# Performance work log

Measured on AMD Instinct MI355X. Metric: run time of the kernel, lower is better.

The kernel has to match this reference:

```python
import jax, jax.numpy as jnp
import numpy as np

B = 8            # graphs per batch
N_PER = 32768    # nodes per graph (equal-size graphs -> trivial to_dense_batch)
N = B * N_PER    # total nodes
DEG = 8
E = N * DEG      # total edges
D = 64           # hidden dim (hard-coded 64 in the module)
K = 16           # num_clusters
NCT = 8          # n_cell_type_groups


def setup_inputs() -> dict:
    key = jax.random.key(0)
    ks = jax.random.split(key, 12)
    # node cell-type indices (x[:,0].long() feeds the embedding)
    x = jax.random.randint(ks[0], (N, 1), 0, NCT, dtype=jnp.int32)
    # within-graph edges: graph id of edge e is e // (E//B)
    epg = E // B
    g = jnp.arange(E, dtype=jnp.int64) // epg
    src = jax.random.randint(ks[1], (E,), 0, N_PER, dtype=jnp.int64) + g * N_PER
    dst = jax.random.randint(ks[2], (E,), 0, N_PER, dtype=jnp.int64) + g * N_PER
    edge_index = jnp.stack([src, dst], axis=0)
    batch = (jnp.arange(N, dtype=jnp.int32) // N_PER).astype(jnp.int32)
    n_cells = jnp.full((B,), float(N_PER), dtype=jnp.float32)
    # parameters
    def lin(k, fi, fo):
        kw, kb = jax.random.split(k)
        lim = 1.0 / np.sqrt(fi)
        return (jax.random.uniform(kw, (fi, fo), jnp.float32, -lim, lim),
                jax.random.uniform(kb, (fo,), jnp.float32, -lim, lim))
    emb_w = jax.random.normal(ks[3], (NCT, D), jnp.float32) * (np.sqrt(6.0 / (NCT + D)) / np.sqrt(3.0))
    W2, b2 = lin(ks[4], D, D)   # conv2 (GCNConv 64->64)
    W3, b3 = lin(ks[5], D, D)   # conv3 (GCNConv 64->64)
    W1, b1 = lin(ks[6], D, K)   # linear1 -> cluster logits
    Wp, bp = lin(ks[7], K, 1)   # linear2 ('prop' head)
    return {"x": x, "edge_index": edge_index, "batch": batch, "n_cells": n_cells,
            "emb_w": emb_w, "W2": W2, "b2": b2, "W3": W3, "b3": b3,
            "W1": W1, "b1": b1, "Wp": Wp, "bp": bp}


def _forward(x, edge_index, batch, n_cells, emb_w, W2, b2, W3, b3, W1, b1, Wp, bp):
    n = x.shape[0]
    h = emb_w[x[:, 0]]                                   # [N, 64] embedding lookup
    src, dst = edge_index[0], edge_index[1]
    # GCN normalization with self-loops
    ar = jnp.arange(n, dtype=src.dtype)
    src_sl = jnp.concatenate([src, ar])
    dst_sl = jnp.concatenate([dst, ar])
    deg = jax.ops.segment_sum(jnp.ones_like(dst_sl, dtype=h.dtype), dst_sl, num_segments=n)
    dis = jax.lax.rsqrt(deg)                             # deg >= 1 (self-loops)
    norm = dis[src_sl] * dis[dst_sl]                     # [E+N]

    def gcn(z, W, b):
        m = z @ W                                        # [N, Dout]
        msg = m[src_sl] * norm[:, None]                  # gather + scale
        return jax.ops.segment_sum(msg, dst_sl, num_segments=n) + b

    # n_gcns == 2, skip_type == 'no'
    out = jax.nn.relu(gcn(h, W2, b2))
    out = jax.nn.relu(gcn(out, W3, b3))
    s = out @ W1 + b1                                    # [N, K] cluster logits
    s_soft = jax.nn.softmax(s, axis=-1)

    # sparse mincut pooling losses
    g_e = batch[src].astype(jnp.int32)                   # graph id per edge
    mincut_num = jax.ops.segment_sum((s_soft[src] * s_soft[dst]).sum(-1), g_e, num_segments=B)
    deg_a = jax.ops.segment_sum(jnp.ones((src.shape[0],), h.dtype), src, num_segments=n)
    mincut_den = jax.ops.segment_sum(deg_a * (s_soft * s_soft).sum(-1), batch, num_segments=B)
    mc1 = jnp.mean(-mincut_num / mincut_den)

    s_b = s_soft.reshape(B, N_PER, K)                    # to_dense_batch (equal graphs)
    SS = jnp.einsum('bnk,bnl->bkl', s_b, s_b)            # [B, K, K]
    ss_norm = jnp.sqrt(jnp.sum(SS * SS, axis=(-2, -1), keepdims=True))
    i_k = jnp.eye(K, dtype=h.dtype) / jnp.sqrt(jnp.asarray(K, h.dtype))
    diff = SS / ss_norm - i_k
    o1 = jnp.mean(jnp.sqrt(jnp.sum(diff * diff, axis=(-2, -1))))

    # predictor_type == 'prop'
    xp = s_b.sum(axis=-2) / n_cells[:, None]             # [B, K]
    pred = xp @ Wp + bp                                  # [B, 1]
    return pred, s_b, mc1, o1


def reference(x, edge_index, batch, n_cells, emb_w, W2, b2, W3, b3, W1, b1, Wp, bp):
    return _forward(x, edge_index, batch, n_cells, emb_w, W2, b2, W3, b3, W1, b1, Wp, bp)
```

## Files before the change

kernel.cpp:

```cpp
#include <hip/hip_runtime.h>
#include <hip/hip_bf16.h>
#include <hip/hip_fp16.h>
#include <math.h>

#define NN 262144
#define EE 2097152
#define NPER 32768
#define EPG 262144
#define EMAX 5120

typedef float4 f4;
typedef __attribute__((ext_vector_type(4))) float f32x4;
typedef __attribute__((ext_vector_type(8))) _Float16 half8;
typedef __attribute__((ext_vector_type(4))) _Float16 half4;

__global__ __launch_bounds__(256) void k_hist(const int* __restrict__ ei, int* __restrict__ histT) {
  __shared__ int histl[64];
  int t = threadIdx.x;
  int bid = blockIdx.x;
  int g = bid & 7, c = bid >> 3;
  if (t < 64) histl[t] = 0;
  __syncthreads();
  int gN = g * NPER;
  const int4* dst4 = (const int4*)(ei + EE + (size_t)g * EPG + c * 4096);
#pragma unroll
  for (int j = 0; j < 4; ++j) {
    int4 d4 = dst4[j * 256 + t];
    atomicAdd(&histl[(d4.x - gN) >> 9], 1);
    atomicAdd(&histl[(d4.y - gN) >> 9], 1);
    atomicAdd(&histl[(d4.z - gN) >> 9], 1);
    atomicAdd(&histl[(d4.w - gN) >> 9], 1);
  }
  __syncthreads();
  if (t < 64) histT[((size_t)g * 64 + t) * 64 + c] = histl[t];
}

__global__ __launch_bounds__(64) void k_hscan(const int* __restrict__ histT, int* __restrict__ winOff,
                                              int* __restrict__ winCnt, int* __restrict__ baseB) {
  int g = blockIdx.x, w = threadIdx.x;
  const int* hrow = histT + ((size_t)g * 64 + w) * 64;
  int tot = 0;
#pragma unroll
  for (int c = 0; c < 64; ++c) tot += hrow[c];
  int incl = tot;
#pragma unroll
  for (int o = 1; o < 64; o <<= 1) {
    int u = __shfl_up(incl, o);
    if (w >= o) incl += u;
  }
  int excl = incl - tot;
  int base = g * EPG + excl;
  winOff[g * 64 + w] = base;
  winCnt[g * 64 + w] = tot;
  int run = base;
  for (int c = 0; c < 64; ++c) {
    baseB[((size_t)g * 64 + c) * 64 + w] = run;
    run += hrow[c];
  }
}

__global__ __launch_bounds__(256) void k_scat(const int* __restrict__ ei, const int* __restrict__ baseB,
                                              int* __restrict__ binned) {
  __shared__ int curl[64];
  int t = threadIdx.x;
  int bid = blockIdx.x;
  int g = bid & 7, c = bid >> 3;
  if (t < 64) curl[t] = baseB[((size_t)g * 64 + c) * 64 + t];
  __syncthreads();
  int gN = g * NPER;
  const int4* src4 = (const int4*)(ei + (size_t)g * EPG + c * 4096);
  const int4* dst4 = (const int4*)(ei + EE + (size_t)g * EPG + c * 4096);
#pragma unroll
  for (int j = 0; j < 4; ++j) {
    int4 s4 = src4[j * 256 + t];
    int4 d4 = dst4[j * 256 + t];
    int dl, w, pos;
    dl = d4.x - gN; w = dl >> 9; pos = atomicAdd(&curl[w], 1); binned[pos] = s4.x | ((dl & 511) << 18);
    dl = d4.y - gN; w = dl >> 9; pos = atomicAdd(&curl[w], 1); binned[pos] = s4.y | ((dl & 511) << 18);
    dl = d4.z - gN; w = dl >> 9; pos = atomicAdd(&curl[w], 1); binned[pos] = s4.z | ((dl & 511) << 18);
    dl = d4.w - gN; w = dl >> 9; pos = atomicAdd(&curl[w], 1); binned[pos] = s4.w | ((dl & 511) << 18);
  }
}

__global__ __launch_bounds__(512) void k_build(const int* __restrict__ binned, const int* __restrict__ winOff,
                                               const int* __restrict__ winCnt, const int* __restrict__ x,
                                               int* __restrict__ offs, int* __restrict__ cnt,
                                               float* __restrict__ dis, float2* __restrict__ dx,
                                               int* __restrict__ adj) {
  __shared__ int ebuf[EMAX];
  __shared__ int cntl[512];
  __shared__ int wsum[8];
  int t = threadIdx.x;
  int bid = blockIdx.x;
  int g = bid & 7, w = bid >> 3;
  int winIdx = g * 64 + w;
  int base = winOff[winIdx];
  int nE = winCnt[winIdx];
  if (nE > EMAX) nE = EMAX;
  for (int i = t; i < nE; i += 512) ebuf[i] = binned[base + i];
  cntl[t] = 0;
  __syncthreads();
  for (int i = t; i < nE; i += 512) atomicAdd(&cntl[ebuf[i] >> 18], 1);
  __syncthreads();
  int c = cntl[t];
  int lane = t & 63, wv = t >> 6;
  int incl = c;
#pragma unroll
  for (int o = 1; o < 64; o <<= 1) {
    int u = __shfl_up(incl, o);
    if (lane >= o) incl += u;
  }
  if (lane == 63) wsum[wv] = incl;
  __syncthreads();
  if (t == 0) {
    int r = 0;
#pragma unroll
    for (int i = 0; i < 8; ++i) { int v = wsum[i]; wsum[i] = r; r += v; }
  }
  __syncthreads();
  int ex = incl - c + wsum[wv];
  int node = g * NPER + w * 512 + t;
  offs[node] = base + ex;
  cnt[node] = c;
  float dn = rsqrtf((float)(c + 1));
  dis[node] = dn;
  dx[node] = make_float2(dn, __int_as_float(x[node]));
  cntl[t] = base + ex;
  __syncthreads();
  for (int i = t; i < nE; i += 512) {
    int v = ebuf[i];
    int pos = atomicAdd(&cntl[v >> 18], 1);
    adj[pos] = v & 0x3FFFF;
  }
}

__global__ void k_m1(const float* __restrict__ emb, const float* __restrict__ W2, float* __restrict__ M1) {
  int t = threadIdx.x;
  int c = t >> 6, j = t & 63;
  float acc = 0.f;
  for (int k = 0; k < 64; ++k) acc += emb[c * 64 + k] * W2[k * 64 + j];
  M1[c * 64 + j] = acc;
}

__global__ __launch_bounds__(256) void k_pack(const float* __restrict__ W3, const float* __restrict__ W1,
                                              _Float16* __restrict__ W3p, _Float16* __restrict__ W1p) {
  int t = blockIdx.x * 256 + threadIdx.x;
  if (t < 4096) {
    int jt = t >> 10, kk = (t >> 9) & 1, l = (t >> 3) & 63, i = t & 7;
    int k = kk * 32 + (l >> 4) * 8 + i;
    int j = jt * 16 + (l & 15);
    W3p[t] = (_Float16)W3[k * 64 + j];
  } else if (t < 5120) {
    int q = t - 4096;
    int kk = q >> 9, l = (q >> 3) & 63, i = q & 7;
    int k = kk * 32 + (l >> 4) * 8 + i;
    int c = l & 15;
    W1p[q] = (_Float16)W1[k * 16 + c];
  }
}

__global__ __launch_bounds__(256) void k_out1(const int* __restrict__ adj, const int* __restrict__ offs,
                                              const int* __restrict__ cnt, const float2* __restrict__ dx,
                                              const float* __restrict__ M1, const float* __restrict__ b2,
                                              __half2* __restrict__ out1h) {
  int tid = threadIdx.x;
  int bid = blockIdx.x;
  int swz = (bid & 7) * 2048 + (bid >> 3);
  int node = swz * 16 + (tid >> 4);
  int t16 = tid & 15;
  float2 dxn = dx[node];
  float dn = dxn.x;
  int xc = __float_as_int(dxn.y);
  int off = offs[node], c = cnt[node];
  float wv[8] = {0.f, 0.f, 0.f, 0.f, 0.f, 0.f, 0.f, 0.f};
  for (int it = t16; it < c; it += 16) {
    int s = adj[off + it];
    float2 v = dx[s];
    int cls = __float_as_int(v.y);
#pragma unroll
    for (int k = 0; k < 8; ++k) wv[k] += (cls == k) ? v.x : 0.f;
  }
#pragma unroll
  for (int k = 0; k < 8; ++k) {
#pragma unroll
    for (int m = 1; m < 16; m <<= 1) wv[k] += __shfl_xor(wv[k], m);
    wv[k] = (wv[k] + ((k == xc) ? dn : 0.f)) * dn;
  }
  int j0 = t16 * 4;
  float o0 = b2[j0], o1 = b2[j0 + 1], o2 = b2[j0 + 2], o3 = b2[j0 + 3];
#pragma unroll
  for (int k = 0; k < 8; ++k) {
    f4 m = *(const f4*)&M1[k * 64 + j0];
    o0 += wv[k] * m.x; o1 += wv[k] * m.y; o2 += wv[k] * m.z; o3 += wv[k] * m.w;
  }
  __half2 h01 = __floats2half2_rn(fmaxf(o0, 0.f) * dn, fmaxf(o1, 0.f) * dn);
  __half2 h23 = __floats2half2_rn(fmaxf(o2, 0.f) * dn, fmaxf(o3, 0.f) * dn);
  size_t p = (size_t)node * 32 + t16 * 2;
  out1h[p] = h01;
  out1h[p + 1] = h23;
}

__global__ __launch_bounds__(256) void k_layer2(const int* __restrict__ adj, const int* __restrict__ offs,
                                                const int* __restrict__ cnt, const float* __restrict__ dis,
                                                const __half2* __restrict__ out1h,
                                                const _Float16* __restrict__ W3p, const float* __restrict__ b3,
                                                const _Float16* __restrict__ W1p, const float* __restrict__ b1,
                                                float* __restrict__ dout) {
  __shared__ _Float16 aggh[16 * 64];
  __shared__ _Float16 o2h[16 * 64];
  int tid = threadIdx.x;
  int bid = blockIdx.x;
  int swz = (bid & 7) * 2048 + (bid >> 3);
  int lane = tid & 63;
  int w = tid >> 6;
  int sub = lane >> 4, part = lane & 15;
  int ndl = (w << 2) + sub;
  int node = swz * 16 + ndl;

  float dn = dis[node];
  int off = offs[node];
  int c = cnt[node];
  const __half2* sp = out1h + (size_t)node * 32 + part * 2;
  float2 f01 = __half22float2(sp[0]), f23 = __half22float2(sp[1]);
  float ax = f01.x, ay = f01.y, az = f23.x, aw = f23.y;
  int it = 0;
  for (; it + 4 <= c; it += 4) {
    int s0 = adj[off + it], s1 = adj[off + it + 1], s2 = adj[off + it + 2], s3 = adj[off + it + 3];
    const __half2* p0 = out1h + (size_t)s0 * 32 + part * 2;
    const __half2* p1 = out1h + (size_t)s1 * 32 + part * 2;
    const __half2* p2 = out1h + (size_t)s2 * 32 + part * 2;
    const __half2* p3 = out1h + (size_t)s3 * 32 + part * 2;
    __half2 a0 = p0[0], c0 = p0[1], a1 = p1[0], c1 = p1[1];
    __half2 a2 = p2[0], c2 = p2[1], a3 = p3[0], c3 = p3[1];
    float2 u;
    u = __half22float2(a0); ax += u.x; ay += u.y;  u = __half22float2(c0); az += u.x; aw += u.y;
    u = __half22float2(a1); ax += u.x; ay += u.y;  u = __half22float2(c1); az += u.x; aw += u.y;
    u = __half22float2(a2); ax += u.x; ay += u.y;  u = __half22float2(c2); az += u.x; aw += u.y;
    u = __half22float2(a3); ax += u.x; ay += u.y;  u = __half22float2(c3); az += u.x; aw += u.y;
  }
  for (; it < c; ++it) {
    int s = adj[off + it];
    const __half2* hp = out1h + (size_t)s * 32 + part * 2;
    float2 g01 = __half22float2(hp[0]), g23 = __half22float2(hp[1]);
    ax += g01.x; ay += g01.y; az += g23.x; aw += g23.y;
  }
  {
    half4 hv = { (_Float16)(dn * ax), (_Float16)(dn * ay), (_Float16)(dn * az), (_Float16)(dn * aw) };
    int byte = (ndl * 128 + part * 8) ^ ((ndl & 7) << 4);
    *(half4*)((char*)aggh + byte) = hv;
  }
  __syncthreads();

  f32x4 acc = {0.f, 0.f, 0.f, 0.f};
#pragma unroll
  for (int kk = 0; kk < 2; ++kk) {
    int row = lane & 15;
    int abyte = (row * 128 + kk * 64 + (lane >> 4) * 16) ^ ((row & 7) << 4);
    half8 afrag = *(const half8*)((const char*)aggh + abyte);
    half8 bfrag = *(const half8*)&W3p[((w * 2 + kk) * 64 + lane) * 8];
    acc = __builtin_amdgcn_mfma_f32_16x16x32_f16(afrag, bfrag, acc, 0, 0, 0);
  }
  {
    int colj = w * 16 + (lane & 15);
    float b3v = b3[colj];
#pragma unroll
    for (int r = 0; r < 4; ++r) {
      int nrow = (lane >> 4) * 4 + r;
      _Float16 hv = (_Float16)fmaxf(acc[r] + b3v, 0.f);
      int byte = (nrow * 128 + colj * 2) ^ ((nrow & 7) << 4);
      *(_Float16*)((char*)o2h + byte) = hv;
    }
  }
  __syncthreads();

  f32x4 acc2 = {0.f, 0.f, 0.f, 0.f};
#pragma unroll
  for (int kk = 0; kk < 2; ++kk) {
    int row = lane & 15;
    int abyte = (row * 128 + kk * 64 + (lane >> 4) * 16) ^ ((row & 7) << 4);
    half8 afrag = *(const half8*)((const char*)o2h + abyte);
    half8 bfrag = *(const half8*)&W1p[(kk * 64 + lane) * 8];
    acc2 = __builtin_amdgcn_mfma_f32_16x16x32_f16(afrag, bfrag, acc2, 0, 0, 0);
  }
  {
    float sv = acc2[w] + b1[lane & 15];
    float mx = sv;
#pragma unroll
    for (int m = 1; m < 16; m <<= 1) mx = fmaxf(mx, __shfl_xor(mx, m));
    float ex = expf(sv - mx);
    float sm = ex;
#pragma unroll
    for (int m = 1; m < 16; m <<= 1) sm += __shfl_xor(sm, m);
    int nrow = (lane >> 4) * 4 + w;
    dout[8 + (size_t)swz * 256 + nrow * 16 + (lane & 15)] = ex / sm;
  }
}

__global__ __launch_bounds__(256) void k_num(const int* __restrict__ adj, const int* __restrict__ offs,
                                             const int* __restrict__ cnt, const float* __restrict__ sb,
                                             float* __restrict__ numP, float* __restrict__ denP) {
  __shared__ float redn[16];
  __shared__ float redd[16];
  int tid = threadIdx.x;
  int bid = blockIdx.x;
  int swz = (bid & 7) * 2048 + (bid >> 3);
  int grp = tid >> 4, t16 = tid & 15;
  int node = swz * 16 + grp;
  int off = offs[node];
  int c = cnt[node];
  float sv = 0.f, sq = 0.f;
  int it = 0;
  for (; it + 4 <= c; it += 4) {
    int s0 = adj[off + it], s1 = adj[off + it + 1], s2 = adj[off + it + 2], s3 = adj[off + it + 3];
    float v0 = sb[(size_t)s0 * 16 + t16];
    float v1 = sb[(size_t)s1 * 16 + t16];
    float v2 = sb[(size_t)s2 * 16 + t16];
    float v3 = sb[(size_t)s3 * 16 + t16];
    sv += v0 + v1 + v2 + v3;
    sq += v0 * v0 + v1 * v1 + v2 * v2 + v3 * v3;
  }
  for (; it < c; ++it) {
    float v = sb[(size_t)adj[off + it] * 16 + t16];
    sv += v;
    sq += v * v;
  }
  float dot = sb[(size_t)node * 16 + t16] * sv;
#pragma unroll
  for (int m = 1; m < 16; m <<= 1) {
    dot += __shfl_xor(dot, m);
    sq  += __shfl_xor(sq, m);
  }
  if (t16 == 0) { redn[grp] = dot; redd[grp] = sq; }
  __syncthreads();
  if (tid == 0) {
    float a = 0.f, b = 0.f;
#pragma unroll
    for (int i = 0; i < 16; ++i) { a += redn[i]; b += redd[i]; }
    numP[swz] = a;
    denP[swz] = b;
  }
}

__global__ __launch_bounds__(256) void k_ssden(const float* __restrict__ sb,
                                               float* __restrict__ xpP, float* __restrict__ SSp) {
  __shared__ float sl[256 * 17];
  __shared__ float xpl[16];
  int t = threadIdx.x;
  int b = blockIdx.x;
  int t1 = t >> 4, t2 = t & 15;
  if (t < 16) xpl[t] = 0.f;
  int node = b * 256 + t;
  const f4* pr = (const f4*)&sb[(size_t)node * 16];
  f4 r0 = pr[0], r1 = pr[1], r2 = pr[2], r3 = pr[3];
  float* row = &sl[t * 17];
  row[0] = r0.x; row[1] = r0.y; row[2] = r0.z; row[3] = r0.w;
  row[4] = r1.x; row[5] = r1.y; row[6] = r1.z; row[7] = r1.w;
  row[8] = r2.x; row[9] = r2.y; row[10] = r2.z; row[11] = r2.w;
  row[12] = r3.x; row[13] = r3.y; row[14] = r3.z; row[15] = r3.w;
  __syncthreads();
  float ss = 0.f;
  for (int n = 0; n < 256; ++n) ss += sl[n * 17 + t1] * sl[n * 17 + t2];
  SSp[(size_t)b * 256 + t] = ss;
  float colsum = 0.f;
#pragma unroll
  for (int r = 0; r < 16; ++r) colsum += sl[(t1 * 16 + r) * 17 + t2];
  atomicAdd(&xpl[t2], colsum);
  __syncthreads();
  if (t < 16) xpP[b * 16 + t] = xpl[t];
}

__global__ __launch_bounds__(256) void k_red(const float* __restrict__ numP, const float* __restrict__ denP,
                                             const float* __restrict__ SSp, const float* __restrict__ xpP,
                                             float* __restrict__ accum) {
  __shared__ float r1[256], r2[256];
  __shared__ float bc;
  int g = blockIdx.x, t = threadIdx.x;
  float acc = 0.f;
  for (int b = 0; b < 128; ++b) acc += SSp[((size_t)(g * 128 + b)) * 256 + t];
  float a = 0.f, d = 0.f;
  for (int i = 0; i < 8; ++i) {
    a += numP[g * 2048 + i * 256 + t];
    d += denP[g * 2048 + i * 256 + t];
  }
  r1[t] = a; r2[t] = d;
  __syncthreads();
  for (int off = 128; off > 0; off >>= 1) {
    if (t < off) { r1[t] += r1[t + off]; r2[t] += r2[t + off]; }
    __syncthreads();
  }
  if (t == 0) { accum[g] = r1[0]; accum[8 + g] = r2[0]; }
  if (t < 16) {
    float s = 0.f;
    for (int b = 0; b < 128; ++b) s += xpP[(g * 128 + b) * 16 + t];
    accum[16 + g * 16 + t] = s;
  }
  __syncthreads();
  r1[t] = acc * acc;
  __syncthreads();
  for (int off = 128; off > 0; off >>= 1) {
    if (t < off) r1[t] += r1[t + off];
    __syncthreads();
  }
  if (t == 0) bc = sqrtf(r1[0]);
  __syncthreads();
  float dv = acc / bc - (((t >> 4) == (t & 15)) ? 0.25f : 0.f);
  r1[t] = dv * dv;
  __syncthreads();
  for (int off = 128; off > 0; off >>= 1) {
    if (t < off) r1[t] += r1[t + off];
    __syncthreads();
  }
  if (t == 0) accum[144 + g] = sqrtf(r1[0]);
}

__global__ __launch_bounds__(64) void k_final(const float* __restrict__ accum, const float* __restrict__ ncells,
                                              const float* __restrict__ Wp, const float* __restrict__ bp,
                                              float* __restrict__ dout) {
  int t = threadIdx.x;
  const float* num = accum;
  const float* den = accum + 8;
  const float* xp  = accum + 16;
  const float* o1g = accum + 144;
  if (t == 0) {
    float m = 0.f, o = 0.f;
    for (int g = 0; g < 8; ++g) { m += -num[g] / den[g]; o += o1g[g]; }
    dout[8 + (size_t)NN * 16] = m / 8.f;
    dout[8 + (size_t)NN * 16 + 1] = o / 8.f;
  }
  if (t < 8) {
    float p = bp[0];
    for (int k = 0; k < 16; ++k) p += (xp[t * 16 + k] / ncells[t]) * Wp[k];
    dout[t] = p;
  }
}

extern "C" void kernel_launch(void* const* d_in, const int* in_sizes, int n_in,
                              void* d_out, int out_size, void* d_ws, size_t ws_size,
                              hipStream_t stream) {
  const int* x            = (const int*)d_in[0];
  const int* ei           = (const int*)d_in[1];
  const float* ncells     = (const float*)d_in[3];
  const float* emb        = (const float*)d_in[4];
  const float* W2         = (const float*)d_in[5];
  const float* b2         = (const float*)d_in[6];
  const float* W3         = (const float*)d_in[7];
  const float* b3         = (const float*)d_in[8];
  const float* W1         = (const float*)d_in[9];
  const float* b1         = (const float*)d_in[10];
  const float* Wp         = (const float*)d_in[11];
  const float* bp         = (const float*)d_in[12];
  float* dout = (float*)d_out;

  char* w = (char*)d_ws;
  float* accum = (float*)w;
  float* dis   = accum + 160;
  float2* dx   = (float2*)(dis + NN);
  int* offs    = (int*)(dx + NN);
  int* cnt     = offs + NN;
  int* adj     = cnt + NN;
  float* M1    = (float*)(adj + EE);
  _Float16* W3p = (_Float16*)(M1 + 512);
  _Float16* W1p = W3p + 4096;
  __half2* out1h = (__half2*)(W1p + 1024);
  float* numP  = (float*)(out1h + (size_t)NN * 32);
  float* denP  = numP + 16384;
  float* SSp   = denP + 16384;
  float* xpP   = SSp + 1024 * 256;
  int* histT   = (int*)(xpP + 1024 * 16);
  int* baseB   = histT + 8 * 64 * 64;
  int* winOff  = baseB + 8 * 64 * 64;
  int* winCnt  = winOff + 512;
  int* binned  = winCnt + 512;

  k_hist  <<<512, 256, 0, stream>>>(ei, histT);
  k_hscan <<<8, 64, 0, stream>>>(histT, winOff, winCnt, baseB);
  k_scat  <<<512, 256, 0, stream>>>(ei, baseB, binned);
  k_build <<<512, 512, 0, stream>>>(binned, winOff, winCnt, x, offs, cnt, dis, dx, adj);
  k_m1    <<<1, 512, 0, stream>>>(emb, W2, M1);
  k_pack  <<<20, 256, 0, stream>>>(W3, W1, W3p, W1p);
  k_out1  <<<16384, 256, 0, stream>>>(adj, offs, cnt, dx, M1, b2, out1h);
  k_layer2<<<16384, 256, 0, stream>>>(adj, offs, cnt, dis, out1h, W3p, b3, W1p, b1, dout);
  k_num   <<<16384, 256, 0, stream>>>(adj, offs, cnt, dout + 8, numP, denP);
  k_ssden <<<1024, 256, 0, stream>>>(dout + 8, xpP, SSp);
  k_red   <<<8, 256, 0, stream>>>(numP, denP, SSp, xpP, accum);
  k_final <<<1, 64, 0, stream>>>(accum, ncells, Wp, bp, dout);
}
```

Before: 269.9 us.

## Fuse prep kernels, window-based layer1, fp16 gathers for layer2 and mincut numerator

Merges the M1 and weight-pack kernels into one launch and replaces the per-node CSR gather in layer 1 with a window kernel that reads binned edges and accumulates per-class weights through shared-memory atomics. Layer 2 now accumulates neighbour features in half2 arithmetic with an 8-way unrolled gather, and also writes a half-precision copy of the soft assignments. The mincut numerator kernel gathers that fp16 copy with 8 lanes per node and 32 nodes per block, roughly halving gather bytes. The intent is fewer launches and less memory traffic, at the cost of reduced precision (fp16 accumulation over neighbours) and shared-memory atomic contention.

```diff
diff --git a/kernel.cpp b/kernel.cpp
--- a/kernel.cpp
+++ b/kernel.cpp
@@ -12,7 +12,6 @@
 typedef float4 f4;
 typedef __attribute__((ext_vector_type(4))) float f32x4;
 typedef __attribute__((ext_vector_type(8))) _Float16 half8;
-typedef __attribute__((ext_vector_type(4))) _Float16 half4;
 
 __global__ __launch_bounds__(256) void k_hist(const int* __restrict__ ei, int* __restrict__ histT) {
   __shared__ int histl[64];
@@ -85,8 +84,7 @@
 __global__ __launch_bounds__(512) void k_build(const int* __restrict__ binned, const int* __restrict__ winOff,
                                                const int* __restrict__ winCnt, const int* __restrict__ x,
                                                int* __restrict__ offs, int* __restrict__ cnt,
-                                               float* __restrict__ dis, float2* __restrict__ dx,
-                                               int* __restrict__ adj) {
+                                               float2* __restrict__ dx, int* __restrict__ adj) {
   __shared__ int ebuf[EMAX];
   __shared__ int cntl[512];
   __shared__ int wsum[8];
@@ -123,7 +121,6 @@
   offs[node] = base + ex;
   cnt[node] = c;
   float dn = rsqrtf((float)(c + 1));
-  dis[node] = dn;
   dx[node] = make_float2(dn, __int_as_float(x[node]));
   cntl[t] = base + ex;
   __syncthreads();
@@ -134,78 +131,84 @@
   }
 }
 
-__global__ void k_m1(const float* __restrict__ emb, const float* __restrict__ W2, float* __restrict__ M1) {
-  int t = threadIdx.x;
-  int c = t >> 6, j = t & 63;
-  float acc = 0.f;
-  for (int k = 0; k < 64; ++k) acc += emb[c * 64 + k] * W2[k * 64 + j];
-  M1[c * 64 + j] = acc;
-}
-
-__global__ __launch_bounds__(256) void k_pack(const float* __restrict__ W3, const float* __restrict__ W1,
-                                              _Float16* __restrict__ W3p, _Float16* __restrict__ W1p) {
-  int t = blockIdx.x * 256 + threadIdx.x;
-  if (t < 4096) {
+__global__ __launch_bounds__(256) void k_prep(const float* __restrict__ emb, const float* __restrict__ W2,
+                                              const float* __restrict__ W3, const float* __restrict__ W1,
+                                              float* __restrict__ M1, _Float16* __restrict__ W3p,
+                                              _Float16* __restrict__ W1p) {
+  int bid = blockIdx.x;
+  int t = bid * 256 + threadIdx.x;
+  if (bid < 16) {
     int jt = t >> 10, kk = (t >> 9) & 1, l = (t >> 3) & 63, i = t & 7;
     int k = kk * 32 + (l >> 4) * 8 + i;
     int j = jt * 16 + (l & 15);
     W3p[t] = (_Float16)W3[k * 64 + j];
-  } else if (t < 5120) {
+  } else if (bid < 20) {
     int q = t - 4096;
     int kk = q >> 9, l = (q >> 3) & 63, i = q & 7;
     int k = kk * 32 + (l >> 4) * 8 + i;
     int c = l & 15;
     W1p[q] = (_Float16)W1[k * 16 + c];
-  }
-}
-
-__global__ __launch_bounds__(256) void k_out1(const int* __restrict__ adj, const int* __restrict__ offs,
-                                              const int* __restrict__ cnt, const float2* __restrict__ dx,
-                                              const float* __restrict__ M1, const float* __restrict__ b2,
-                                              __half2* __restrict__ out1h) {
-  int tid = threadIdx.x;
-  int bid = blockIdx.x;
-  int swz = (bid & 7) * 2048 + (bid >> 3);
-  int node = swz * 16 + (tid >> 4);
-  int t16 = tid & 15;
+  } else {
+    int idx = t - 5120;
+    int c = idx >> 6, j = idx & 63;
+    float acc = 0.f;
+    for (int k = 0; k < 64; ++k) acc += emb[c * 64 + k] * W2[k * 64 + j];
+    M1[idx] = acc;
+  }
+}
+
+__global__ __launch_bounds__(512) void k_wout1(const int* __restrict__ binned, const int* __restrict__ winOff,
+                                               const int* __restrict__ winCnt, const float2* __restrict__ dx,
+                                               const float* __restrict__ M1, const float* __restrict__ b2,
+                                               __half2* __restrict__ out1h) {
+  __shared__ float w8l[512 * 8];
+  int t = threadIdx.x;
+  int bid = blockIdx.x;
+  int g = bid & 7, w = bid >> 3;
+  int winIdx = g * 64 + w;
+  int base = winOff[winIdx];
+  int nE = winCnt[winIdx];
+#pragma unroll
+  for (int i = 0; i < 8; ++i) w8l[i * 512 + t] = 0.f;
+  __syncthreads();
+  for (int i = t; i < nE; i += 512) {
+    int v = binned[base + i];
+    int s = v & 0x3FFFF;
+    int dl = v >> 18;
+    float2 sv = dx[s];
+    atomicAdd(&w8l[dl * 8 + __float_as_int(sv.y)], sv.x);
+  }
+  __syncthreads();
+  int node = g * NPER + w * 512 + t;
   float2 dxn = dx[node];
   float dn = dxn.x;
   int xc = __float_as_int(dxn.y);
-  int off = offs[node], c = cnt[node];
-  float wv[8] = {0.f, 0.f, 0.f, 0.f, 0.f, 0.f, 0.f, 0.f};
-  for (int it = t16; it < c; it += 16) {
-    int s = adj[off + it];
-    float2 v = dx[s];
-    int cls = __float_as_int(v.y);
-#pragma unroll
-    for (int k = 0; k < 8; ++k) wv[k] += (cls == k) ? v.x : 0.f;
-  }
-#pragma unroll
-  for (int k = 0; k < 8; ++k) {
-#pragma unroll
-    for (int m = 1; m < 16; m <<= 1) wv[k] += __shfl_xor(wv[k], m);
-    wv[k] = (wv[k] + ((k == xc) ? dn : 0.f)) * dn;
-  }
-  int j0 = t16 * 4;
-  float o0 = b2[j0], o1 = b2[j0 + 1], o2 = b2[j0 + 2], o3 = b2[j0 + 3];
-#pragma unroll
-  for (int k = 0; k < 8; ++k) {
-    f4 m = *(const f4*)&M1[k * 64 + j0];
-    o0 += wv[k] * m.x; o1 += wv[k] * m.y; o2 += wv[k] * m.z; o3 += wv[k] * m.w;
-  }
-  __half2 h01 = __floats2half2_rn(fmaxf(o0, 0.f) * dn, fmaxf(o1, 0.f) * dn);
-  __half2 h23 = __floats2half2_rn(fmaxf(o2, 0.f) * dn, fmaxf(o3, 0.f) * dn);
-  size_t p = (size_t)node * 32 + t16 * 2;
-  out1h[p] = h01;
-  out1h[p + 1] = h23;
+  float wv[8];
+#pragma unroll
+  for (int c = 0; c < 8; ++c) wv[c] = (w8l[t * 8 + c] + ((c == xc) ? dn : 0.f)) * dn;
+  __half2 orow[32];
+#pragma unroll
+  for (int j2 = 0; j2 < 32; ++j2) {
+    float oa = b2[j2 * 2], ob = b2[j2 * 2 + 1];
+#pragma unroll
+    for (int c = 0; c < 8; ++c) {
+      oa += wv[c] * M1[c * 64 + j2 * 2];
+      ob += wv[c] * M1[c * 64 + j2 * 2 + 1];
+    }
+    orow[j2] = __floats2half2_rn(fmaxf(oa, 0.f) * dn, fmaxf(ob, 0.f) * dn);
+  }
+  f4* dstp = (f4*)(out1h + (size_t)node * 32);
+  const f4* srcp = (const f4*)orow;
+#pragma unroll
+  for (int q = 0; q < 8; ++q) dstp[q] = srcp[q];
 }
 
 __global__ __launch_bounds__(256) void k_layer2(const int* __restrict__ adj, const int* __restrict__ offs,
-                                                const int* __restrict__ cnt, const float* __restrict__ dis,
+                                                const int* __restrict__ cnt, const float2* __restrict__ dx,
                                                 const __half2* __restrict__ out1h,
                                                 const _Float16* __restrict__ W3p, const float* __restrict__ b3,
                                                 const _Float16* __restrict__ W1p, const float* __restrict__ b1,
-                                                float* __restrict__ dout) {
+                                                float* __restrict__ dout, __half* __restrict__ sbh) {
   __shared__ _Float16 aggh[16 * 64];
   __shared__ _Float16 o2h[16 * 64];
   int tid = threadIdx.x;
@@ -217,37 +220,37 @@
   int ndl = (w << 2) + sub;
   int node = swz * 16 + ndl;
 
-  float dn = dis[node];
+  float dn = dx[node].x;
   int off = offs[node];
   int c = cnt[node];
-  const __half2* sp = out1h + (size_t)node * 32 + part * 2;
-  float2 f01 = __half22float2(sp[0]), f23 = __half22float2(sp[1]);
-  float ax = f01.x, ay = f01.y, az = f23.x, aw = f23.y;
+  const __half2* sp = out1h + ((size_t)node << 5) + (part << 1);
+  __half2 a01 = sp[0], a23 = sp[1];
   int it = 0;
-  for (; it + 4 <= c; it += 4) {
-    int s0 = adj[off + it], s1 = adj[off + it + 1], s2 = adj[off + it + 2], s3 = adj[off + it + 3];
-    const __half2* p0 = out1h + (size_t)s0 * 32 + part * 2;
-    const __half2* p1 = out1h + (size_t)s1 * 32 + part * 2;
-    const __half2* p2 = out1h + (size_t)s2 * 32 + part * 2;
-    const __half2* p3 = out1h + (size_t)s3 * 32 + part * 2;
-    __half2 a0 = p0[0], c0 = p0[1], a1 = p1[0], c1 = p1[1];
-    __half2 a2 = p2[0], c2 = p2[1], a3 = p3[0], c3 = p3[1];
-    float2 u;
-    u = __half22float2(a0); ax += u.x; ay += u.y;  u = __half22float2(c0); az += u.x; aw += u.y;
-    u = __half22float2(a1); ax += u.x; ay += u.y;  u = __half22float2(c1); az += u.x; aw += u.y;
-    u = __half22float2(a2); ax += u.x; ay += u.y;  u = __half22float2(c2); az += u.x; aw += u.y;
-    u = __half22float2(a3); ax += u.x; ay += u.y;  u = __half22float2(c3); az += u.x; aw += u.y;
+  for (; it + 8 <= c; it += 8) {
+    int sA[8];
+#pragma unroll
+    for (int u = 0; u < 8; ++u) sA[u] = adj[off + it + u];
+#pragma unroll
+    for (int u = 0; u < 8; ++u) {
+      const __half2* hp = out1h + (((size_t)sA[u]) << 5) + (part << 1);
+      __half2 h0 = hp[0], h1 = hp[1];
+      a01 = __hadd2(a01, h0);
+      a23 = __hadd2(a23, h1);
+    }
   }
   for (; it < c; ++it) {
-    int s = adj[off + it];
-    const __half2* hp = out1h + (size_t)s * 32 + part * 2;
-    float2 g01 = __half22float2(hp[0]), g23 = __half22float2(hp[1]);
-    ax += g01.x; ay += g01.y; az += g23.x; aw += g23.y;
+    const __half2* hp = out1h + (((size_t)adj[off + it]) << 5) + (part << 1);
+    __half2 h0 = hp[0], h1 = hp[1];
+    a01 = __hadd2(a01, h0);
+    a23 = __hadd2(a23, h1);
   }
   {
-    half4 hv = { (_Float16)(dn * ax), (_Float16)(dn * ay), (_Float16)(dn * az), (_Float16)(dn * aw) };
+    __half2 dn2 = __float2half2_rn(dn);
+    a01 = __hmul2(a01, dn2);
+    a23 = __hmul2(a23, dn2);
     int byte = (ndl * 128 + part * 8) ^ ((ndl & 7) << 4);
-    *(half4*)((char*)aggh + byte) = hv;
+    *(__half2*)((char*)aggh + byte) = a01;
+    *(__half2*)((char*)aggh + byte + 4) = a23;
   }
   __syncthreads();
 
@@ -291,53 +294,58 @@
     float sm = ex;
 #pragma unroll
     for (int m = 1; m < 16; m <<= 1) sm += __shfl_xor(sm, m);
+    float so = ex / sm;
     int nrow = (lane >> 4) * 4 + w;
-    dout[8 + (size_t)swz * 256 + nrow * 16 + (lane & 15)] = ex / sm;
+    dout[8 + (size_t)swz * 256 + nrow * 16 + (lane & 15)] = so;
+    sbh[((swz * 16 + nrow) << 4) + (lane & 15)] = __float2half(so);
   }
 }
 
 __global__ __launch_bounds__(256) void k_num(const int* __restrict__ adj, const int* __restrict__ offs,
-                                             const int* __restrict__ cnt, const float* __restrict__ sb,
+                                             const int* __restrict__ cnt, const __half2* __restrict__ sbh2,
                                              float* __restrict__ numP, float* __restrict__ denP) {
-  __shared__ float redn[16];
-  __shared__ float redd[16];
+  __shared__ float redn[32];
+  __shared__ float redd[32];
   int tid = threadIdx.x;
   int bid = blockIdx.x;
-  int swz = (bid & 7) * 2048 + (bid >> 3);
-  int grp = tid >> 4, t16 = tid & 15;
-  int node = swz * 16 + grp;
+  int swz = (bid & 7) * 1024 + (bid >> 3);
+  int grp = tid >> 3, t8 = tid & 7;
+  int node = swz * 32 + grp;
   int off = offs[node];
   int c = cnt[node];
-  float sv = 0.f, sq = 0.f;
+  float svx = 0.f, svy = 0.f, sq = 0.f;
   int it = 0;
-  for (; it + 4 <= c; it += 4) {
-    int s0 = adj[off + it], s1 = adj[off + it + 1], s2 = adj[off + it + 2], s3 = adj[off + it + 3];
-    float v0 = sb[(size_t)s0 * 16 + t16];
-    float v1 = sb[(size_t)s1 * 16 + t16];
-    float v2 = sb[(size_t)s2 * 16 + t16];
-    float v3 = sb[(size_t)s3 * 16 + t16];
-    sv += v0 + v1 + v2 + v3;
-    sq += v0 * v0 + v1 * v1 + v2 * v2 + v3 * v3;
+  for (; it + 8 <= c; it += 8) {
+    int sA[8];
+#pragma unroll
+    for (int u = 0; u < 8; ++u) sA[u] = adj[off + it + u];
+#pragma unroll
+    for (int u = 0; u < 8; ++u) {
+      float2 v = __half22float2(sbh2[(sA[u] << 3) + t8]);
+      svx += v.x; svy += v.y; sq += v.x * v.x + v.y * v.y;
+    }
   }
   for (; it < c; ++it) {
-    float v = sb[(size_t)adj[off + it] * 16 + t16];
-    sv += v;
-    sq += v * v;
-  }
-  float dot = sb[(size_t)node * 16 + t16] * sv;
-#pragma unroll
-  for (int m = 1; m < 16; m <<= 1) {
+    float2 v = __half22float2(sbh2[(adj[off + it] << 3) + t8]);
+    svx += v.x; svy += v.y; sq += v.x * v.x + v.y * v.y;
+  }
+  float2 sf = __half22float2(sbh2[(node << 3) + t8]);
+  float dot = sf.x * svx + sf.y * svy;
+#pragma unroll
+  for (int m = 1; m < 8; m <<= 1) {
     dot += __shfl_xor(dot, m);
     sq  += __shfl_xor(sq, m);
   }
-  if (t16 == 0) { redn[grp] = dot; redd[grp] = sq; }
-  __syncthreads();
-  if (tid == 0) {
-    float a = 0.f, b = 0.f;
-#pragma unroll
-    for (int i = 0; i < 16; ++i) { a += redn[i]; b += redd[i]; }
-    numP[swz] = a;
-    denP[swz] = b;
+  if (t8 == 0) { redn[grp] = dot; redd[grp] = sq; }
+  __syncthreads();
+  if (tid < 32) {
+    float a = redn[tid], d = redd[tid];
+#pragma unroll
+    for (int m = 1; m < 32; m <<= 1) {
+      a += __shfl_xor(a, m);
+      d += __shfl_xor(d, m);
+    }
+    if (tid == 0) { numP[swz] = a; denP[swz] = d; }
   }
 }
 
@@ -378,9 +386,9 @@
   float acc = 0.f;
   for (int b = 0; b < 128; ++b) acc += SSp[((size_t)(g * 128 + b)) * 256 + t];
   float a = 0.f, d = 0.f;
-  for (int i = 0; i < 8; ++i) {
-    a += numP[g * 2048 + i * 256 + t];
-    d += denP[g * 2048 + i * 256 + t];
+  for (int i = 0; i < 4; ++i) {
+    a += numP[g * 1024 + i * 256 + t];
+    d += denP[g * 1024 + i * 256 + t];
   }
   r1[t] = a; r2[t] = d;
   __syncthreads();
@@ -453,8 +461,7 @@
 
   char* w = (char*)d_ws;
   float* accum = (float*)w;
-  float* dis   = accum + 160;
-  float2* dx   = (float2*)(dis + NN);
+  float2* dx   = (float2*)(accum + 160);
   int* offs    = (int*)(dx + NN);
   int* cnt     = offs + NN;
   int* adj     = cnt + NN;
@@ -462,9 +469,10 @@
   _Float16* W3p = (_Float16*)(M1 + 512);
   _Float16* W1p = W3p + 4096;
   __half2* out1h = (__half2*)(W1p + 1024);
-  float* numP  = (float*)(out1h + (size_t)NN * 32);
-  float* denP  = numP + 16384;
-  float* SSp   = denP + 16384;
+  __half* sbh  = (__half*)(out1h + (size_t)NN * 32);
+  float* numP  = (float*)(sbh + (size_t)NN * 16);
+  float* denP  = numP + 8192;
+  float* SSp   = denP + 8192;
   float* xpP   = SSp + 1024 * 256;
   int* histT   = (int*)(xpP + 1024 * 16);
   int* baseB   = histT + 8 * 64 * 64;
@@ -475,12 +483,11 @@
   k_hist  <<<512, 256, 0, stream>>>(ei, histT);
   k_hscan <<<8, 64, 0, stream>>>(histT, winOff, winCnt, baseB);
   k_scat  <<<512, 256, 0, stream>>>(ei, baseB, binned);
-  k_build <<<512, 512, 0, stream>>>(binned, winOff, winCnt, x, offs, cnt, dis, dx, adj);
-  k_m1    <<<1, 512, 0, stream>>>(emb, W2, M1);
-  k_pack  <<<20, 256, 0, stream>>>(W3, W1, W3p, W1p);
-  k_out1  <<<16384, 256, 0, stream>>>(adj, offs, cnt, dx, M1, b2, out1h);
-  k_layer2<<<16384, 256, 0, stream>>>(adj, offs, cnt, dis, out1h, W3p, b3, W1p, b1, dout);
-  k_num   <<<16384, 256, 0, stream>>>(adj, offs, cnt, dout + 8, numP, denP);
+  k_build <<<512, 512, 0, stream>>>(binned, winOff, winCnt, x, offs, cnt, dx, adj);
+  k_prep  <<<22, 256, 0, stream>>>(emb, W2, W3, W1, M1, W3p, W1p);
+  k_wout1 <<<512, 512, 0, stream>>>(binned, winOff, winCnt, dx, M1, b2, out1h);
+  k_layer2<<<16384, 256, 0, stream>>>(adj, offs, cnt, dx, out1h, W3p, b3, W1p, b1, dout, sbh);
+  k_num   <<<8192, 256, 0, stream>>>(adj, offs, cnt, (const __half2*)sbh, numP, denP);
   k_ssden <<<1024, 256, 0, stream>>>(dout + 8, xpP, SSp);
   k_red   <<<8, 256, 0, stream>>>(numP, denP, SSp, xpP, accum);
   k_final <<<1, 64, 0, stream>>>(accum, ncells, Wp, bp, dout);
```

After: 269.2 us. No clear change (-0.3%).
